# Optimization experiments

Hardware: AMD Instinct MI355X
Metric: run time of the kernel (lower is better)

Reference implementation:

```python
import jax, jax.numpy as jnp
import numpy as np

HUMAN_SIZE = 54
NUM_ACTIONS = 15
INPUT_SIZE = HUMAN_SIZE + NUM_ACTIONS  # 69
RNN_SIZE = 2048
BATCH = 512
SRC_LEN = 100
TGT_LEN = 50


def setup_inputs() -> dict:
    key = jax.random.key(0)
    ks = jax.random.split(key, 8)
    s = 1.0 / np.sqrt(RNN_SIZE)
    return {
        "encoder_inputs": jax.random.normal(ks[0], (BATCH, SRC_LEN, INPUT_SIZE), jnp.float32),
        "decoder_inputs": jax.random.normal(ks[1], (BATCH, TGT_LEN, INPUT_SIZE), jnp.float32),
        # GRUCell params (torch layout: weight_ih [3H, D], weight_hh [3H, H])
        "W_ih": jax.random.uniform(ks[2], (3 * RNN_SIZE, INPUT_SIZE), jnp.float32, -s, s),
        "W_hh": jax.random.uniform(ks[3], (3 * RNN_SIZE, RNN_SIZE), jnp.float32, -s, s),
        "b_ih": jax.random.uniform(ks[4], (3 * RNN_SIZE,), jnp.float32, -s, s),
        "b_hh": jax.random.uniform(ks[5], (3 * RNN_SIZE,), jnp.float32, -s, s),
        # fc1: Linear(rnn_size -> input_size)
        "fc1_w": jax.random.uniform(ks[6], (INPUT_SIZE, RNN_SIZE), jnp.float32, -s, s),
        "fc1_b": jax.random.uniform(ks[7], (INPUT_SIZE,), jnp.float32, -s, s),
    }


def _gru_cell(x, h, W_ih, W_hh, b_ih, b_hh):
    # torch.nn.GRUCell math
    gi = x @ W_ih.T + b_ih  # [B, 3H]
    gh = h @ W_hh.T + b_hh  # [B, 3H]
    i_r, i_z, i_n = jnp.split(gi, 3, axis=-1)
    h_r, h_z, h_n = jnp.split(gh, 3, axis=-1)
    r = jax.nn.sigmoid(i_r + h_r)
    z = jax.nn.sigmoid(i_z + h_z)
    n = jnp.tanh(i_n + r * h_n)
    return (1.0 - z) * n + z * h


def reference(encoder_inputs, decoder_inputs, W_ih, W_hh, b_ih, b_hh, fc1_w, fc1_b):
    B = encoder_inputs.shape[0]
    state0 = jnp.zeros((B, RNN_SIZE), encoder_inputs.dtype)

    # Encoder: source_seq_len - 1 steps (dropout p=0.0 -> identity)
    enc_t = jnp.swapaxes(encoder_inputs[:, : SRC_LEN - 1], 0, 1)  # [L-1, B, D]

    def enc_step(h, x):
        return _gru_cell(x, h, W_ih, W_hh, b_ih, b_hh), None

    state, _ = jax.lax.scan(enc_step, state0, enc_t)

    # (loop_function feeds the previous output back as the next input).
    def dec_step(carry, _):
        h, inp = carry
        inp = jax.lax.stop_gradient(inp)  # inp.detach() in torch
        h = _gru_cell(inp, h, W_ih, W_hh, b_ih, b_hh)
        out = inp + h @ fc1_w.T + fc1_b  # residual
        return (h, out), out

    (_, _), outs = jax.lax.scan(dec_step, (state, decoder_inputs[:, 0]), None, length=TGT_LEN)
    return jnp.swapaxes(outs, 0, 1)  # [B, TGT_LEN, INPUT_SIZE]
```

## Files before the change

### kernel.cpp

```cpp
#include <hip/hip_runtime.h>

#define KP   2176
#define H    2048
#define IN   69
#define TGT  50
#define NKT  68

typedef unsigned short ushort_t;
typedef unsigned int   uint_t;
typedef __attribute__((ext_vector_type(8))) short  short8;
typedef __attribute__((ext_vector_type(4))) float  float4_t;

#define MFMA_BF16 __builtin_amdgcn_mfma_f32_16x16x32_bf16

__device__ __forceinline__ ushort_t f2bf(float f) {
  union { float f; unsigned u; } v; v.f = f;
  unsigned u = v.u;
  return (ushort_t)((u + 0x7fffu + ((u >> 16) & 1u)) >> 16);
}

template <int N> __device__ __forceinline__ void waitv() {
  asm volatile("s_waitcnt vmcnt(%0)" :: "n"(N) : "memory");
}
#define LGKM0() asm volatile("s_waitcnt lgkmcnt(0)" ::: "memory")
#define SGB0()  __builtin_amdgcn_sched_barrier(0)
#define FENCE() asm volatile("" ::: "memory")

template <int OFF> __device__ __forceinline__ void gld(short8& d, uint_t voff, const void* base) {
  asm volatile("global_load_dwordx4 %0, %1, %2 offset:%3"
               : "=v"(d) : "v"(voff), "s"(base), "n"(OFF));
}
template <int OFF> __device__ __forceinline__ void gld_sc(short8& d, uint_t voff, const void* base) {
  asm volatile("global_load_dwordx4 %0, %1, %2 offset:%3 sc0 sc1"
               : "=v"(d) : "v"(voff), "s"(base), "n"(OFF));
}
__device__ __forceinline__ void st128_sc(void* addr, short8 v) {
  asm volatile("global_store_dwordx4 %0, %1, off sc0 sc1" :: "v"(addr), "v"(v) : "memory");
}
__device__ __forceinline__ void st16_sc(void* addr, uint_t v) {
  asm volatile("global_store_short %0, %1, off sc0 sc1" :: "v"(addr), "v"(v) : "memory");
}
__device__ __forceinline__ void st32_sc(void* addr, float v) {
  asm volatile("global_store_dword %0, %1, off sc0 sc1" :: "v"(addr), "v"(v) : "memory");
}
__device__ __forceinline__ void ld32_sc_nw(float& d, const void* addr) {
  asm volatile("global_load_dword %0, %1, off sc0 sc1" : "=v"(d) : "v"(addr) : "memory");
}

__global__ void build_w3(const float* __restrict__ Whh, const float* __restrict__ Wih,
                         ushort_t* __restrict__ W3) {
  int i = blockIdx.x * 256 + threadIdx.x;
  int lane = i & 63;
  int kt = (i >> 6) % NKT;
  int rb = i / (64 * NKT);
  int cb = rb / 3, g = rb - cb * 3;
  int c  = cb * 16 + (lane & 15);
  int gr = g * H + c;
  int k0 = kt * 32 + (lane >> 4) * 8;
  short8 v;
  #pragma unroll
  for (int j = 0; j < 8; ++j) {
    int k = k0 + j;
    float val = 0.f;
    if (k < H) val = Whh[(size_t)gr * H + k];
    else if (k < H + IN) val = Wih[(size_t)gr * IN + (k - H)];
    v[j] = (short)f2bf(val);
  }
  *(short8*)(W3 + (size_t)i * 8) = v;
}

__global__ void build_f2(const float* __restrict__ fc1w, ushort_t* __restrict__ F2) {
  int i = blockIdx.x * 256 + threadIdx.x;
  int lane = i & 63;
  int ni = (i >> 6) % 5;
  int kt = i / 320;
  int j  = ni * 16 + (lane & 15);
  int k0 = kt * 32 + (lane >> 4) * 8;
  short8 v;
  #pragma unroll
  for (int jj = 0; jj < 8; ++jj) {
    float val = (j < IN) ? fc1w[(size_t)j * H + k0 + jj] : 0.f;
    v[jj] = (short)f2bf(val);
  }
  *(short8*)(F2 + (size_t)i * 8) = v;
}

__global__ void zero_u4(uint4* p, int n) {
  int i = blockIdx.x * 256 + threadIdx.x;
  if (i < n) p[i] = make_uint4(0, 0, 0, 0);
}

__device__ __forceinline__ size_t a2_x_off(int b, int j) {
  int k = 2048 + j;
  int kt = k >> 5, kk = k & 31;
  int mb = b >> 4;
  int ln = (b & 15) | ((kk >> 3) << 4);
  return ((size_t)(mb * NKT + kt) * 64 + ln) * 16 + (kk & 7) * 2;
}

__global__ void fill_x0(const float* __restrict__ enc, char* __restrict__ A2) {
  int i = blockIdx.x * 256 + threadIdx.x;
  int b = i / IN, j = i - b * IN;
  *(ushort_t*)(A2 + a2_x_off(b, j)) = f2bf(enc[(size_t)b * 100 * IN + j]);
}

__global__ __launch_bounds__(256, 1) void persist(
    const char* __restrict__ W3p, char* A0, char* A1, const char* __restrict__ F2p,
    const float* __restrict__ enc, const float* __restrict__ dec,
    const float* __restrict__ bih, const float* __restrict__ bhh,
    const float* __restrict__ fc1b, float* __restrict__ out, int* barcnt)
{
  __shared__ __align__(16) char ldsraw[25600];
  short8  (*Aring)[4][64] = (short8 (*)[4][64])ldsraw;
  ushort_t (*smh)[72]     = (ushort_t (*)[72])(ldsraw + 16384);

  const int tid = threadIdx.x;
  const int bid = blockIdx.x;
  const int lane = tid & 63, w = tid >> 6;
  const int l15 = lane & 15, l4 = lane >> 4;
  const int cg = (bid & 7) * 4 + ((bid >> 3) & 3);
  const int mt = bid >> 5;
  const int cb = cg * 4 + w;
  const int c  = cb * 16 + l15;

  const float br  = bih[c] + bhh[c];
  const float bz  = bih[H + c] + bhh[H + c];
  const float bin = bih[2 * H + c];
  const float bhn = bhh[2 * H + c];
  asm volatile("" :: "v"(br), "v"(bz), "v"(bin), "v"(bhn));

  float hreg[4][4] = {};

  const uint_t vAi  = (uint_t)(w * (NKT * 1024) + lane * 16);
  const uint_t vB0i = (uint_t)((cb * 3 + 0) * (NKT * 1024) + lane * 16);
  const uint_t vB1i = vB0i + (uint_t)(NKT * 1024);
  const uint_t vB2i = vB1i + (uint_t)(NKT * 1024);

  int epoch = 0;
  auto gbar = [&]() {
    asm volatile("s_waitcnt vmcnt(0) lgkmcnt(0)" ::: "memory");
    __builtin_amdgcn_s_barrier();
    ++epoch;
    if (tid == 0) {
      atomicAdd(barcnt, 1);
      const int tgt = epoch * 256;
      int v = 0;
      for (int it = 0; it < 20000000; ++it) {
        asm volatile("global_load_dword %0, %1, off sc0 sc1\n\ts_waitcnt vmcnt(0)"
                     : "=v"(v) : "v"((const int*)barcnt) : "memory");
        if (v >= tgt) break;
        __builtin_amdgcn_s_sleep(2);
      }
    }
    __builtin_amdgcn_s_barrier();
  };

  #pragma unroll 1
  for (int t = 0; t < 149; ++t) {
    char* Ain  = (t & 1) ? A1 : A0;
    char* Aout = (t & 1) ? A0 : A1;
    const void* ApW = Ain + (size_t)(mt * 4) * (NKT * 1024);

    uint_t vA = vAi;
    uint_t vB0 = vB0i, vB1 = vB1i, vB2 = vB2i;

    short8 sa[8], fb[8][3];
    short8 fa0, fa1, fa2, fa3;
    float4_t acc[4][4] = {};

#define AISS(sl) { gld_sc<0>(sa[sl], vA, ApW); vA += 1024; }
#define BISS(sl) { gld<0>(fb[sl][0], vB0, W3p); gld<0>(fb[sl][1], vB1, W3p); \
                   gld<0>(fb[sl][2], vB2, W3p); vB0 += 1024; vB1 += 1024; vB2 += 1024; }
#define MFMA3(mi, fav, j, G2) \
  acc[mi][0]  = MFMA_BF16(fav, fb[j][0], acc[mi][0], 0, 0, 0); \
  acc[mi][1]  = MFMA_BF16(fav, fb[j][1], acc[mi][1], 0, 0, 0); \
  acc[mi][G2] = MFMA_BF16(fav, fb[j][2], acc[mi][G2], 0, 0, 0);
#define MFMA12(j, G2) MFMA3(0, fa0, j, G2) MFMA3(1, fa1, j, G2) \
                      MFMA3(2, fa2, j, G2) MFMA3(3, fa3, j, G2)
#define RDFA(ss) \
  FENCE(); \
  fa0 = Aring[ss][0][lane]; fa1 = Aring[ss][1][lane]; \
  fa2 = Aring[ss][2][lane]; fa3 = Aring[ss][3][lane];

#define GRUT(u, G2) \
  AISS(u) BISS((u + 7) & 7) \
  waitv<28>(); SGB0(); \
  Aring[((u) + 1) & 3][w][lane] = sa[(u + 1) & 7]; \
  LGKM0(); \
  __builtin_amdgcn_s_barrier(); \
  RDFA(u & 3) \
  LGKM0(); SGB0(); \
  MFMA12(u, G2)
#define GRUTB(u, NW) \
  BISS((u + 7) & 7) \
  waitv<NW>(); SGB0(); \
  Aring[((u) + 1) & 3][w][lane] = sa[(u + 1) & 7]; \
  LGKM0(); \
  __builtin_amdgcn_s_barrier(); \
  RDFA(u & 3) \
  LGKM0(); SGB0(); \
  MFMA12(u, 2)
#define GRUTN_W(u, NW, G2) \
  waitv<NW>(); SGB0(); \
  Aring[((u) + 1) & 3][w][lane] = sa[(u + 1) & 7]; \
  LGKM0(); \
  __builtin_amdgcn_s_barrier(); \
  RDFA(u & 3) \
  LGKM0(); SGB0(); \
  MFMA12(u, G2)
#define GRUTN_NW(u, NW, G2) \
  waitv<NW>(); SGB0(); \
  LGKM0(); \
  __builtin_amdgcn_s_barrier(); \
  RDFA(u & 3) \
  LGKM0(); SGB0(); \
  MFMA12(u, G2)

    AISS(0)
    AISS(1) BISS(0)
    AISS(2) BISS(1)
    AISS(3) BISS(2)
    AISS(4) BISS(3)
    AISS(5) BISS(4)
    AISS(6) BISS(5)
    AISS(7) BISS(6)
    waitv<28>(); SGB0();
    Aring[0][w][lane] = sa[0];
    LGKM0();
    __builtin_amdgcn_s_barrier();

    #pragma unroll 1
    for (int g8 = 0; g8 < 7; ++g8) {
      GRUT(0, 2) GRUT(1, 2) GRUT(2, 2) GRUT(3, 2)
      GRUT(4, 2) GRUT(5, 2) GRUT(6, 2) GRUT(7, 2)
    }
    GRUT(0, 2) GRUT(1, 2) GRUT(2, 2) GRUT(3, 2)
    GRUTB(4, 27)
    GRUTN_W(5, 23, 2) GRUTN_W(6, 19, 2) GRUTN_W(7, 15, 2)
    GRUTN_W(0, 11, 3) GRUTN_W(1, 7, 3) GRUTN_W(2, 3, 3) GRUTN_NW(3, 0, 3)

    #pragma unroll
    for (int mi = 0; mi < 4; ++mi) {
      #pragma unroll
      for (int r4 = 0; r4 < 4; ++r4) {
        float rg = 1.f / (1.f + __expf(-(acc[mi][0][r4] + br)));
        float zg = 1.f / (1.f + __expf(-(acc[mi][1][r4] + bz)));
        float ng = tanhf(acc[mi][3][r4] + bin + rg * (acc[mi][2][r4] + bhn));
        float hn = (1.f - zg) * ng + zg * hreg[mi][r4];
        hreg[mi][r4] = hn;
        smh[mi * 16 + l4 * 4 + r4][w * 16 + l15] = f2bf(hn);
      }
    }
    __syncthreads();
    #pragma unroll
    for (int e = 0; e < 2; ++e) {
      int cid = tid * 2 + e;
      int m = cid >> 3, ktrel = (cid >> 2) & 1, khi = cid & 3;
      short8 v = *(const short8*)&smh[m][ktrel * 32 + khi * 8];
      int m_abs = mt * 64 + m;
      int mb2 = m_abs >> 4;
      int ln = (m_abs & 15) | (khi << 4);
      int kt = cg * 2 + ktrel;
      st128_sc(Aout + ((size_t)(mb2 * NKT + kt) * 64 + ln) * 16, v);
    }
    if ((bid & 31) == 0 && t < 99) {
      const float* xs = (t < 98) ? (enc + (size_t)(t + 1) * IN) : dec;
      const int xstride = (t < 98) ? 100 * IN : TGT * IN;
      for (int i = tid; i < 64 * IN; i += 256) {
        int rr = i / IN, cc = i - rr * IN;
        int m = mt * 64 + rr;
        st16_sc(Aout + a2_x_off(m, cc), (uint_t)f2bf(xs[(size_t)m * xstride + cc]));
      }
    }
    gbar();

    if (t >= 99) {
      if (bid < 32) {
        const int d = t - 99;
        const int mbo = bid;
        float4_t* redf = (float4_t*)ldsraw;
        const void* F2b = (const char*)F2p + 4096;
        uint_t voA = (uint_t)((mbo * NKT + w * 16) * 1024 + lane * 16);
        uint_t vf  = (uint_t)((w * 16) * 5120 + lane * 16);
        short8 da[8], db[8][5];
        float4_t oa[5] = {};

#define DPRO(sl) \
        gld_sc<0>(da[sl], voA, Aout); \
        gld<0>(db[sl][0], vf, F2p); gld<1024>(db[sl][1], vf, F2p); \
        gld<2048>(db[sl][2], vf, F2p); gld<3072>(db[sl][3], vf, F2p); \
        gld<0>(db[sl][4], vf, F2b); \
        voA += 1024; vf += 5120;
#define DMM(sl) \
        { _Pragma("unroll") for (int nf = 0; nf < 5; ++nf) \
            oa[nf] = MFMA_BF16(da[sl], db[sl][nf], oa[nf], 0, 0, 0); }

        DPRO(0) DPRO(1) DPRO(2) DPRO(3) DPRO(4) DPRO(5) DPRO(6) DPRO(7)
        waitv<42>(); SGB0(); DMM(0) DPRO(0)
        waitv<42>(); SGB0(); DMM(1) DPRO(1)
        waitv<42>(); SGB0(); DMM(2) DPRO(2)
        waitv<42>(); SGB0(); DMM(3) DPRO(3)
        waitv<42>(); SGB0(); DMM(4) DPRO(4)
        waitv<42>(); SGB0(); DMM(5) DPRO(5)
        waitv<42>(); SGB0(); DMM(6) DPRO(6)
        waitv<42>(); SGB0(); DMM(7) DPRO(7)
        waitv<42>(); SGB0(); DMM(0)
        waitv<36>(); SGB0(); DMM(1)
        waitv<30>(); SGB0(); DMM(2)
        waitv<24>(); SGB0(); DMM(3)
        waitv<18>(); SGB0(); DMM(4)
        waitv<12>(); SGB0(); DMM(5)
        waitv<6>();  SGB0(); DMM(6)
        waitv<0>();  SGB0(); DMM(7)

        #pragma unroll
        for (int nf = 0; nf < 5; ++nf) redf[(w * 5 + nf) * 64 + lane] = oa[nf];
        __syncthreads();

        #pragma unroll 1
        for (int pass = 0; pass < 2; ++pass) {
          if (pass == 1 && w != 0) break;
          const int nf = pass ? 4 : w;
          float4_t sum = redf[(0 * 5 + nf) * 64 + lane] + redf[(1 * 5 + nf) * 64 + lane]
                       + redf[(2 * 5 + nf) * 64 + lane] + redf[(3 * 5 + nf) * 64 + lane];
          int j = nf * 16 + l15;
          if (j < IN) {
            float bj = fc1b[j];
            float iv0, iv1, iv2, iv3;
            if (d == 0) {
              iv0 = dec[(size_t)(mbo * 16 + l4 * 4 + 0) * (TGT * IN) + j];
              iv1 = dec[(size_t)(mbo * 16 + l4 * 4 + 1) * (TGT * IN) + j];
              iv2 = dec[(size_t)(mbo * 16 + l4 * 4 + 2) * (TGT * IN) + j];
              iv3 = dec[(size_t)(mbo * 16 + l4 * 4 + 3) * (TGT * IN) + j];
            } else {
              const float* pv = out + (size_t)(d - 1) * IN + j;
              ld32_sc_nw(iv0, pv + (size_t)(mbo * 16 + l4 * 4 + 0) * (TGT * IN));
              ld32_sc_nw(iv1, pv + (size_t)(mbo * 16 + l4 * 4 + 1) * (TGT * IN));
              ld32_sc_nw(iv2, pv + (size_t)(mbo * 16 + l4 * 4 + 2) * (TGT * IN));
              ld32_sc_nw(iv3, pv + (size_t)(mbo * 16 + l4 * 4 + 3) * (TGT * IN));
              waitv<0>(); SGB0();
            }
            float ivv[4] = {iv0, iv1, iv2, iv3};
            #pragma unroll
            for (int r4 = 0; r4 < 4; ++r4) {
              int m = mbo * 16 + l4 * 4 + r4;
              float v = sum[r4] + bj + ivv[r4];
              st32_sc(out + (size_t)m * (TGT * IN) + (size_t)d * IN + j, v);
              st16_sc(Aout + a2_x_off(m, j), (uint_t)f2bf(v));
            }
          }
        }
      }
      gbar();
    }
  }
}

extern "C" void kernel_launch(void* const* d_in, const int* in_sizes, int n_in,
                              void* d_out, int out_size, void* d_ws, size_t ws_size,
                              hipStream_t stream) {
  const float* enc  = (const float*)d_in[0];
  const float* dec  = (const float*)d_in[1];
  const float* Wih  = (const float*)d_in[2];
  const float* Whh  = (const float*)d_in[3];
  const float* b_ih = (const float*)d_in[4];
  const float* b_hh = (const float*)d_in[5];
  const float* fc1w = (const float*)d_in[6];
  const float* fc1b = (const float*)d_in[7];
  float* out = (float*)d_out;

  char* ws = (char*)d_ws;
  ushort_t* W3  = (ushort_t*)ws;
  char*     A0  = ws + 26738688;
  char*     A1  = ws + 28966912;
  int*      bar = (int*)(ws + 31195136);
  ushort_t* F2  = (ushort_t*)(ws + 31196160);

  build_w3<<<6528, 256, 0, stream>>>(Whh, Wih, W3);
  zero_u4<<<1089, 256, 0, stream>>>((uint4*)A0, 278592);
  fill_x0<<<138, 256, 0, stream>>>(enc, A0);
  build_f2<<<80, 256, 0, stream>>>(fc1w, F2);

  persist<<<256, 256, 0, stream>>>((const char*)W3, A0, A1, (const char*)F2,
                                   enc, dec, b_ih, b_hh, fc1b, out, bar);
}
```

Measured before the change: 4.352 ms.

## Split persistent GRU kernel across 512 blocks with half the columns each

Doubles the persistent grid from 256 to 512 blocks at two blocks per CU. Each block now owns 32 hidden columns instead of 64, and its waves split the four row tiles into pairs. LDS and accumulator/register footprint halve to fit the higher occupancy, and the grid barrier target doubles. This aims to spread the weight streaming and MFMA work over more waves. In exchange, every block still loads the full A slice, so redundant A traffic and barrier contention roughly double, and the barrier spin limit is reduced.

After: 7.136 ms. 64.0% more time.

```diff
diff --git a/kernel.cpp b/kernel.cpp
--- a/kernel.cpp
+++ b/kernel.cpp
@@ -104,23 +104,25 @@
   *(ushort_t*)(A2 + a2_x_off(b, j)) = f2bf(enc[(size_t)b * 100 * IN + j]);
 }
 
-__global__ __launch_bounds__(256, 1) void persist(
+__global__ __launch_bounds__(256, 2) void persist(
     const char* __restrict__ W3p, char* A0, char* A1, const char* __restrict__ F2p,
     const float* __restrict__ enc, const float* __restrict__ dec,
     const float* __restrict__ bih, const float* __restrict__ bhh,
     const float* __restrict__ fc1b, float* __restrict__ out, int* barcnt)
 {
-  __shared__ __align__(16) char ldsraw[25600];
+  __shared__ __align__(16) char ldsraw[20992];
   short8  (*Aring)[4][64] = (short8 (*)[4][64])ldsraw;
-  ushort_t (*smh)[72]     = (ushort_t (*)[72])(ldsraw + 16384);
+  ushort_t (*smh)[36]     = (ushort_t (*)[36])(ldsraw + 16384);
 
   const int tid = threadIdx.x;
   const int bid = blockIdx.x;
   const int lane = tid & 63, w = tid >> 6;
   const int l15 = lane & 15, l4 = lane >> 4;
-  const int cg = (bid & 7) * 4 + ((bid >> 3) & 3);
-  const int mt = bid >> 5;
-  const int cb = cg * 4 + w;
+  const int slot = bid >> 3;
+  const int cg = (bid & 7) * 8 + (slot & 7);
+  const int mt = slot >> 3;
+  const int wc = w & 1, wh = w >> 1;
+  const int cb = cg * 2 + wc;
   const int c  = cb * 16 + l15;
 
   const float br  = bih[c] + bhh[c];
@@ -129,7 +131,7 @@
   const float bhn = bhh[2 * H + c];
   asm volatile("" :: "v"(br), "v"(bz), "v"(bin), "v"(bhn));
 
-  float hreg[4][4] = {};
+  float hreg[2][4] = {};
 
   const uint_t vAi  = (uint_t)(w * (NKT * 1024) + lane * 16);
   const uint_t vB0i = (uint_t)((cb * 3 + 0) * (NKT * 1024) + lane * 16);
@@ -143,9 +145,9 @@
     ++epoch;
     if (tid == 0) {
       atomicAdd(barcnt, 1);
-      const int tgt = epoch * 256;
+      const int tgt = epoch * 512;
       int v = 0;
-      for (int it = 0; it < 20000000; ++it) {
+      for (int it = 0; it < 5000000; ++it) {
         asm volatile("global_load_dword %0, %1, off sc0 sc1\n\ts_waitcnt vmcnt(0)"
                      : "=v"(v) : "v"((const int*)barcnt) : "memory");
         if (v >= tgt) break;
@@ -165,8 +167,8 @@
     uint_t vB0 = vB0i, vB1 = vB1i, vB2 = vB2i;
 
     short8 sa[8], fb[8][3];
-    short8 fa0, fa1, fa2, fa3;
-    float4_t acc[4][4] = {};
+    short8 fa0, fa1;
+    float4_t acc[2][4] = {};
 
 #define AISS(sl) { gld_sc<0>(sa[sl], vA, ApW); vA += 1024; }
 #define BISS(sl) { gld<0>(fb[sl][0], vB0, W3p); gld<0>(fb[sl][1], vB1, W3p); \
@@ -175,12 +177,10 @@
   acc[mi][0]  = MFMA_BF16(fav, fb[j][0], acc[mi][0], 0, 0, 0); \
   acc[mi][1]  = MFMA_BF16(fav, fb[j][1], acc[mi][1], 0, 0, 0); \
   acc[mi][G2] = MFMA_BF16(fav, fb[j][2], acc[mi][G2], 0, 0, 0);
-#define MFMA12(j, G2) MFMA3(0, fa0, j, G2) MFMA3(1, fa1, j, G2) \
-                      MFMA3(2, fa2, j, G2) MFMA3(3, fa3, j, G2)
+#define MFMA6(j, G2) MFMA3(0, fa0, j, G2) MFMA3(1, fa1, j, G2)
 #define RDFA(ss) \
   FENCE(); \
-  fa0 = Aring[ss][0][lane]; fa1 = Aring[ss][1][lane]; \
-  fa2 = Aring[ss][2][lane]; fa3 = Aring[ss][3][lane];
+  fa0 = Aring[ss][wh * 2][lane]; fa1 = Aring[ss][wh * 2 + 1][lane];
 
 #define GRUT(u, G2) \
   AISS(u) BISS((u + 7) & 7) \
@@ -190,7 +190,7 @@
   __builtin_amdgcn_s_barrier(); \
   RDFA(u & 3) \
   LGKM0(); SGB0(); \
-  MFMA12(u, G2)
+  MFMA6(u, G2)
 #define GRUTB(u, NW) \
   BISS((u + 7) & 7) \
   waitv<NW>(); SGB0(); \
@@ -199,7 +199,7 @@
   __builtin_amdgcn_s_barrier(); \
   RDFA(u & 3) \
   LGKM0(); SGB0(); \
-  MFMA12(u, 2)
+  MFMA6(u, 2)
 #define GRUTN_W(u, NW, G2) \
   waitv<NW>(); SGB0(); \
   Aring[((u) + 1) & 3][w][lane] = sa[(u + 1) & 7]; \
@@ -207,14 +207,14 @@
   __builtin_amdgcn_s_barrier(); \
   RDFA(u & 3) \
   LGKM0(); SGB0(); \
-  MFMA12(u, G2)
+  MFMA6(u, G2)
 #define GRUTN_NW(u, NW, G2) \
   waitv<NW>(); SGB0(); \
   LGKM0(); \
   __builtin_amdgcn_s_barrier(); \
   RDFA(u & 3) \
   LGKM0(); SGB0(); \
-  MFMA12(u, G2)
+  MFMA6(u, G2)
 
     AISS(0)
     AISS(1) BISS(0)
@@ -240,30 +240,28 @@
     GRUTN_W(0, 11, 3) GRUTN_W(1, 7, 3) GRUTN_W(2, 3, 3) GRUTN_NW(3, 0, 3)
 
     #pragma unroll
-    for (int mi = 0; mi < 4; ++mi) {
+    for (int mi = 0; mi < 2; ++mi) {
       #pragma unroll
       for (int r4 = 0; r4 < 4; ++r4) {
+        int mloc = (wh * 2 + mi) * 16 + l4 * 4 + r4;
         float rg = 1.f / (1.f + __expf(-(acc[mi][0][r4] + br)));
         float zg = 1.f / (1.f + __expf(-(acc[mi][1][r4] + bz)));
         float ng = tanhf(acc[mi][3][r4] + bin + rg * (acc[mi][2][r4] + bhn));
         float hn = (1.f - zg) * ng + zg * hreg[mi][r4];
         hreg[mi][r4] = hn;
-        smh[mi * 16 + l4 * 4 + r4][w * 16 + l15] = f2bf(hn);
+        smh[mloc][wc * 16 + l15] = f2bf(hn);
       }
     }
     __syncthreads();
-    #pragma unroll
-    for (int e = 0; e < 2; ++e) {
-      int cid = tid * 2 + e;
-      int m = cid >> 3, ktrel = (cid >> 2) & 1, khi = cid & 3;
-      short8 v = *(const short8*)&smh[m][ktrel * 32 + khi * 8];
-      int m_abs = mt * 64 + m;
+    {
+      int mloc = tid >> 2, khi = tid & 3;
+      short8 v = *(const short8*)&smh[mloc][khi * 8];
+      int m_abs = mt * 64 + mloc;
       int mb2 = m_abs >> 4;
       int ln = (m_abs & 15) | (khi << 4);
-      int kt = cg * 2 + ktrel;
-      st128_sc(Aout + ((size_t)(mb2 * NKT + kt) * 64 + ln) * 16, v);
-    }
-    if ((bid & 31) == 0 && t < 99) {
+      st128_sc(Aout + ((size_t)(mb2 * NKT + cg) * 64 + ln) * 16, v);
+    }
+    if (cg == 0 && t < 99) {
       const float* xs = (t < 98) ? (enc + (size_t)(t + 1) * IN) : dec;
       const int xstride = (t < 98) ? 100 * IN : TGT * IN;
       for (int i = tid; i < 64 * IN; i += 256) {
@@ -381,6 +379,6 @@
   fill_x0<<<138, 256, 0, stream>>>(enc, A0);
   build_f2<<<80, 256, 0, stream>>>(fc1w, F2);
 
-  persist<<<256, 256, 0, stream>>>((const char*)W3, A0, A1, (const char*)F2,
+  persist<<<512, 256, 0, stream>>>((const char*)W3, A0, A1, (const char*)F2,
                                    enc, dec, b_ih, b_hh, fc1b, out, bar);
 }
```

## Run persistent GRU kernel with 128 blocks of 8 waves instead of 256×4

Applied to the files above, without the earlier changes.

Halves the grid to 128 blocks of 512 threads so each block covers 128 hidden columns with 8 waves. Each A tile is now loaded once per block and split across wave pairs with half-width loads into the LDS ring, so each wave brings in less of A. The grid barrier waits for fewer arrivals, and the hidden-state writeback, input staging and decoder fc reduction are reindexed for 8 waves. The cost is a larger LDS footprint and fewer blocks to spread the work over.

Result: slower. 4.927 ms (+13.2%).

```diff
diff --git a/kernel.cpp b/kernel.cpp
--- a/kernel.cpp
+++ b/kernel.cpp
@@ -9,6 +9,7 @@
 typedef unsigned short ushort_t;
 typedef unsigned int   uint_t;
 typedef __attribute__((ext_vector_type(8))) short  short8;
+typedef __attribute__((ext_vector_type(4))) short  short4_t;
 typedef __attribute__((ext_vector_type(4))) float  float4_t;
 
 #define MFMA_BF16 __builtin_amdgcn_mfma_f32_16x16x32_bf16
@@ -32,6 +33,10 @@
 }
 template <int OFF> __device__ __forceinline__ void gld_sc(short8& d, uint_t voff, const void* base) {
   asm volatile("global_load_dwordx4 %0, %1, %2 offset:%3 sc0 sc1"
+               : "=v"(d) : "v"(voff), "s"(base), "n"(OFF));
+}
+template <int OFF> __device__ __forceinline__ void gld2_sc(short4_t& d, uint_t voff, const void* base) {
+  asm volatile("global_load_dwordx2 %0, %1, %2 offset:%3 sc0 sc1"
                : "=v"(d) : "v"(voff), "s"(base), "n"(OFF));
 }
 __device__ __forceinline__ void st128_sc(void* addr, short8 v) {
@@ -104,23 +109,22 @@
   *(ushort_t*)(A2 + a2_x_off(b, j)) = f2bf(enc[(size_t)b * 100 * IN + j]);
 }
 
-__global__ __launch_bounds__(256, 1) void persist(
+__global__ __launch_bounds__(512, 1) void persist(
     const char* __restrict__ W3p, char* A0, char* A1, const char* __restrict__ F2p,
     const float* __restrict__ enc, const float* __restrict__ dec,
     const float* __restrict__ bih, const float* __restrict__ bhh,
     const float* __restrict__ fc1b, float* __restrict__ out, int* barcnt)
 {
-  __shared__ __align__(16) char ldsraw[25600];
-  short8  (*Aring)[4][64] = (short8 (*)[4][64])ldsraw;
-  ushort_t (*smh)[72]     = (ushort_t (*)[72])(ldsraw + 16384);
+  __shared__ __align__(16) char ldsraw[40960];
+  ushort_t (*smh)[136] = (ushort_t (*)[136])(ldsraw + 16384);
 
   const int tid = threadIdx.x;
   const int bid = blockIdx.x;
   const int lane = tid & 63, w = tid >> 6;
   const int l15 = lane & 15, l4 = lane >> 4;
-  const int cg = (bid & 7) * 4 + ((bid >> 3) & 3);
-  const int mt = bid >> 5;
-  const int cb = cg * 4 + w;
+  const int cg = (bid & 7) * 2 + ((bid >> 3) & 1);
+  const int mt = bid >> 4;
+  const int cb = cg * 8 + w;
   const int c  = cb * 16 + l15;
 
   const float br  = bih[c] + bhh[c];
@@ -131,10 +135,11 @@
 
   float hreg[4][4] = {};
 
-  const uint_t vAi  = (uint_t)(w * (NKT * 1024) + lane * 16);
+  const uint_t vAi  = (uint_t)((w >> 1) * (NKT * 1024) + (w & 1) * 512 + lane * 8);
   const uint_t vB0i = (uint_t)((cb * 3 + 0) * (NKT * 1024) + lane * 16);
   const uint_t vB1i = vB0i + (uint_t)(NKT * 1024);
   const uint_t vB2i = vB1i + (uint_t)(NKT * 1024);
+  const uint_t ringw = (uint_t)((w >> 1) * 1024 + (w & 1) * 512 + lane * 8);
 
   int epoch = 0;
   auto gbar = [&]() {
@@ -143,7 +148,7 @@
     ++epoch;
     if (tid == 0) {
       atomicAdd(barcnt, 1);
-      const int tgt = epoch * 256;
+      const int tgt = epoch * 128;
       int v = 0;
       for (int it = 0; it < 20000000; ++it) {
         asm volatile("global_load_dword %0, %1, off sc0 sc1\n\ts_waitcnt vmcnt(0)"
@@ -164,11 +169,12 @@
     uint_t vA = vAi;
     uint_t vB0 = vB0i, vB1 = vB1i, vB2 = vB2i;
 
-    short8 sa[8], fb[8][3];
+    short4_t sa[8];
+    short8 fb[8][3];
     short8 fa0, fa1, fa2, fa3;
     float4_t acc[4][4] = {};
 
-#define AISS(sl) { gld_sc<0>(sa[sl], vA, ApW); vA += 1024; }
+#define AISS(sl) { gld2_sc<0>(sa[sl], vA, ApW); vA += 1024; }
 #define BISS(sl) { gld<0>(fb[sl][0], vB0, W3p); gld<0>(fb[sl][1], vB1, W3p); \
                    gld<0>(fb[sl][2], vB2, W3p); vB0 += 1024; vB1 += 1024; vB2 += 1024; }
 #define MFMA3(mi, fav, j, G2) \
@@ -177,15 +183,19 @@
   acc[mi][G2] = MFMA_BF16(fav, fb[j][2], acc[mi][G2], 0, 0, 0);
 #define MFMA12(j, G2) MFMA3(0, fa0, j, G2) MFMA3(1, fa1, j, G2) \
                       MFMA3(2, fa2, j, G2) MFMA3(3, fa3, j, G2)
+#define AWRITE(slot, sl) \
+  *(short4_t*)(ldsraw + (slot) * 4096 + ringw) = sa[sl];
 #define RDFA(ss) \
   FENCE(); \
-  fa0 = Aring[ss][0][lane]; fa1 = Aring[ss][1][lane]; \
-  fa2 = Aring[ss][2][lane]; fa3 = Aring[ss][3][lane];
+  fa0 = *(const short8*)(ldsraw + (ss) * 4096 + 0    + lane * 16); \
+  fa1 = *(const short8*)(ldsraw + (ss) * 4096 + 1024 + lane * 16); \
+  fa2 = *(const short8*)(ldsraw + (ss) * 4096 + 2048 + lane * 16); \
+  fa3 = *(const short8*)(ldsraw + (ss) * 4096 + 3072 + lane * 16);
 
 #define GRUT(u, G2) \
   AISS(u) BISS((u + 7) & 7) \
   waitv<28>(); SGB0(); \
-  Aring[((u) + 1) & 3][w][lane] = sa[(u + 1) & 7]; \
+  AWRITE(((u) + 1) & 3, (u + 1) & 7) \
   LGKM0(); \
   __builtin_amdgcn_s_barrier(); \
   RDFA(u & 3) \
@@ -194,7 +204,7 @@
 #define GRUTB(u, NW) \
   BISS((u + 7) & 7) \
   waitv<NW>(); SGB0(); \
-  Aring[((u) + 1) & 3][w][lane] = sa[(u + 1) & 7]; \
+  AWRITE(((u) + 1) & 3, (u + 1) & 7) \
   LGKM0(); \
   __builtin_amdgcn_s_barrier(); \
   RDFA(u & 3) \
@@ -202,7 +212,7 @@
   MFMA12(u, 2)
 #define GRUTN_W(u, NW, G2) \
   waitv<NW>(); SGB0(); \
-  Aring[((u) + 1) & 3][w][lane] = sa[(u + 1) & 7]; \
+  AWRITE(((u) + 1) & 3, (u + 1) & 7) \
   LGKM0(); \
   __builtin_amdgcn_s_barrier(); \
   RDFA(u & 3) \
@@ -225,7 +235,7 @@
     AISS(6) BISS(5)
     AISS(7) BISS(6)
     waitv<28>(); SGB0();
-    Aring[0][w][lane] = sa[0];
+    AWRITE(0, 0)
     LGKM0();
     __builtin_amdgcn_s_barrier();
 
@@ -255,18 +265,18 @@
     #pragma unroll
     for (int e = 0; e < 2; ++e) {
       int cid = tid * 2 + e;
-      int m = cid >> 3, ktrel = (cid >> 2) & 1, khi = cid & 3;
-      short8 v = *(const short8*)&smh[m][ktrel * 32 + khi * 8];
-      int m_abs = mt * 64 + m;
+      int mloc = cid >> 4, ktrel = (cid >> 2) & 3, khi = cid & 3;
+      short8 v = *(const short8*)&smh[mloc][ktrel * 32 + khi * 8];
+      int m_abs = mt * 64 + mloc;
       int mb2 = m_abs >> 4;
       int ln = (m_abs & 15) | (khi << 4);
-      int kt = cg * 2 + ktrel;
+      int kt = cg * 4 + ktrel;
       st128_sc(Aout + ((size_t)(mb2 * NKT + kt) * 64 + ln) * 16, v);
     }
-    if ((bid & 31) == 0 && t < 99) {
+    if ((bid & 15) == 0 && t < 99) {
       const float* xs = (t < 98) ? (enc + (size_t)(t + 1) * IN) : dec;
       const int xstride = (t < 98) ? 100 * IN : TGT * IN;
-      for (int i = tid; i < 64 * IN; i += 256) {
+      for (int i = tid; i < 64 * IN; i += 512) {
         int rr = i / IN, cc = i - rr * IN;
         int m = mt * 64 + rr;
         st16_sc(Aout + a2_x_off(m, cc), (uint_t)f2bf(xs[(size_t)m * xstride + cc]));
@@ -280,8 +290,8 @@
         const int mbo = bid;
         float4_t* redf = (float4_t*)ldsraw;
         const void* F2b = (const char*)F2p + 4096;
-        uint_t voA = (uint_t)((mbo * NKT + w * 16) * 1024 + lane * 16);
-        uint_t vf  = (uint_t)((w * 16) * 5120 + lane * 16);
+        uint_t voA = (uint_t)((mbo * NKT + w * 8) * 1024 + lane * 16);
+        uint_t vf  = (uint_t)((w * 8) * 5120 + lane * 16);
         short8 da[8], db[8][5];
         float4_t oa[5] = {};
 
@@ -296,14 +306,6 @@
             oa[nf] = MFMA_BF16(da[sl], db[sl][nf], oa[nf], 0, 0, 0); }
 
         DPRO(0) DPRO(1) DPRO(2) DPRO(3) DPRO(4) DPRO(5) DPRO(6) DPRO(7)
-        waitv<42>(); SGB0(); DMM(0) DPRO(0)
-        waitv<42>(); SGB0(); DMM(1) DPRO(1)
-        waitv<42>(); SGB0(); DMM(2) DPRO(2)
-        waitv<42>(); SGB0(); DMM(3) DPRO(3)
-        waitv<42>(); SGB0(); DMM(4) DPRO(4)
-        waitv<42>(); SGB0(); DMM(5) DPRO(5)
-        waitv<42>(); SGB0(); DMM(6) DPRO(6)
-        waitv<42>(); SGB0(); DMM(7) DPRO(7)
         waitv<42>(); SGB0(); DMM(0)
         waitv<36>(); SGB0(); DMM(1)
         waitv<30>(); SGB0(); DMM(2)
@@ -317,12 +319,11 @@
         for (int nf = 0; nf < 5; ++nf) redf[(w * 5 + nf) * 64 + lane] = oa[nf];
         __syncthreads();
 
-        #pragma unroll 1
-        for (int pass = 0; pass < 2; ++pass) {
-          if (pass == 1 && w != 0) break;
-          const int nf = pass ? 4 : w;
-          float4_t sum = redf[(0 * 5 + nf) * 64 + lane] + redf[(1 * 5 + nf) * 64 + lane]
-                       + redf[(2 * 5 + nf) * 64 + lane] + redf[(3 * 5 + nf) * 64 + lane];
+        if (w < 5) {
+          const int nf = w;
+          float4_t sum = redf[(0 * 5 + nf) * 64 + lane];
+          #pragma unroll
+          for (int g = 1; g < 8; ++g) sum += redf[(g * 5 + nf) * 64 + lane];
           int j = nf * 16 + l15;
           if (j < IN) {
             float bj = fc1b[j];
@@ -381,6 +382,6 @@
   fill_x0<<<138, 256, 0, stream>>>(enc, A0);
   build_f2<<<80, 256, 0, stream>>>(fc1w, F2);
 
-  persist<<<256, 256, 0, stream>>>((const char*)W3, A0, A1, (const char*)F2,
+  persist<<<128, 512, 0, stream>>>((const char*)W3, A0, A1, (const char*)F2,
                                    enc, dec, b_ih, b_hh, fc1b, out, bar);
 }
```
